# Optimization experiments

Measured on AMD Instinct MI355X. Metric: run time of the kernel, lower is better.

The kernel has to match this reference:

```python
import jax, jax.numpy as jnp
import numpy as np

N, E, D_IN, D_H, D_OUT = 100000, 1600000, 128, 128, 47
BN_EPS = 1e-5


def setup_inputs() -> dict:
    key = jax.random.key(0)
    ks = jax.random.split(key, 12)
    x = jax.random.normal(ks[0], (N, D_IN), dtype=jnp.float32)
    edge_index = jax.random.randint(ks[1], (2, E), 0, N, dtype=jnp.int64)
    s = 1.0 / np.sqrt(D_H)
    return {
        "x": x,
        "edge_index": edge_index,
        "W1": jax.random.normal(ks[2], (D_IN, D_H), dtype=jnp.float32) * s,
        "b1": jnp.zeros((D_H,), dtype=jnp.float32),
        "gamma": jax.random.uniform(ks[3], (D_H,), dtype=jnp.float32, minval=0.5, maxval=1.5),
        "beta": jax.random.normal(ks[4], (D_H,), dtype=jnp.float32) * 0.1,
        "mean": jax.random.normal(ks[5], (D_H,), dtype=jnp.float32) * 0.1,
        "var": jax.random.uniform(ks[6], (D_H,), dtype=jnp.float32, minval=0.5, maxval=1.5),
        "W2": jax.random.normal(ks[7], (D_H, D_H), dtype=jnp.float32) * s,
        "b2": jnp.zeros((D_H,), dtype=jnp.float32),
        "Wf": jax.random.normal(ks[8], (D_H, D_OUT), dtype=jnp.float32) * s,
        "bf": jnp.zeros((D_OUT,), dtype=jnp.float32),
    }


def gcn_conv(x, src, dst, W, b, n):
    # x' = x @ W, then symmetric-normalized aggregation with self-loops (PyG GCNConv).
    h = x @ W
    loops = jnp.arange(n, dtype=src.dtype)
    s = jnp.concatenate([src, loops])
    d = jnp.concatenate([dst, loops])
    deg = jax.ops.segment_sum(jnp.ones_like(d, dtype=h.dtype), d, num_segments=n)
    dinv = jnp.where(deg > 0, jax.lax.rsqrt(deg), 0.0)
    norm = dinv[s] * dinv[d]                      # [E+N]
    msg = h[s] * norm[:, None]                    # [E+N, D] gather
    out = jax.ops.segment_sum(msg, d, num_segments=n)  # scatter-add
    return out + b


def reference(x, edge_index, W1, b1, gamma, beta, mean, var, W2, b2, Wf, bf):
    n = x.shape[0]
    src, dst = edge_index[0], edge_index[1]
    # layer 1: GCNConv -> BatchNorm (eval) -> ReLU -> dropout (identity in eval)
    h1 = gcn_conv(x, src, dst, W1, b1, n)
    h1 = (h1 - mean) * jax.lax.rsqrt(var + BN_EPS) * gamma + beta
    h1 = jax.nn.relu(h1)
    # layer 2 (last conv, no BN/act)
    h2 = gcn_conv(h1, src, dst, W2, b2, n)
    # JumpingKnowledge max over layer outputs
    jk = jnp.maximum(h1, h2)
    logits = jk @ Wf + bf
    return jax.nn.log_softmax(logits, axis=1)
```

## Files before the change

kernel.cpp:

```cpp
#include <hip/hip_runtime.h>
#include <math.h>

#define DH 128
#define DOUT 47
#define BN_EPS 1e-5f

#define NCH 64
#define RS 32768
#define RSH 15

typedef __attribute__((ext_vector_type(8))) short short8;
typedef __attribute__((ext_vector_type(4))) float float4v;
typedef __attribute__((ext_vector_type(2))) float float2v;

__device__ __forceinline__ unsigned bf16_rne(float f) {
    unsigned u = __float_as_uint(f);
    return (u + 0x7fffu + ((u >> 16) & 1u)) >> 16;
}
__device__ __forceinline__ unsigned pack_bf2(float a, float b) {
    return (bf16_rne(a) & 0xffffu) | (bf16_rne(b) << 16);
}
__device__ __forceinline__ float2 unpack_bf2(unsigned u) {
    return make_float2(__uint_as_float(u << 16),
                       __uint_as_float(u & 0xffff0000u));
}


__global__ __launch_bounds__(256) void prep_k(const float* __restrict__ W1,
                                              const float* __restrict__ W2,
                                              unsigned* __restrict__ W1b,
                                              unsigned* __restrict__ W2b,
                                              unsigned* __restrict__ bufA, int n) {
    int tid = threadIdx.x;
    const float* W = blockIdx.x ? W2 : W1;
    unsigned* Wb = blockIdx.x ? W2b : W1b;
    if (blockIdx.x == 0 && tid < 64) bufA[(size_t)n * 64 + tid] = 0;
    for (int p = tid; p < 128 * 32; p += 256) {
        int nn = p >> 5;
        int k0 = (p & 31) << 2;
        float f0 = W[(size_t)(k0 + 0) * 128 + nn];
        float f1 = W[(size_t)(k0 + 1) * 128 + nn];
        float f2 = W[(size_t)(k0 + 2) * 128 + nn];
        float f3 = W[(size_t)(k0 + 3) * 128 + nn];
        uint2 v;
        v.x = pack_bf2(f0, f1);
        v.y = pack_bf2(f2, f3);
        *(uint2*)(Wb + (size_t)nn * 64 + (k0 >> 1)) = v;
    }
}

__global__ __launch_bounds__(256) void hist_rank_k(const int* __restrict__ dst,
                                                   int* __restrict__ rank,
                                                   int* __restrict__ cntM,
                                                   int e, int ce, int nr,
                                                   size_t nsp) {
    __shared__ int bins[RS];
    int tid = threadIdx.x;
    int r = blockIdx.x % nr;
    int ch = blockIdx.x / nr;
    {
        int4* b4 = (int4*)bins;
        for (int j = tid; j < RS / 4; j += 256) b4[j] = make_int4(0, 0, 0, 0);
    }
    __syncthreads();
    int lo = ch * ce;
    int hi = lo + ce;
    if (hi > e) hi = e;
    if (lo < hi) {
        int n4end = lo + ((hi - lo) & ~3);
        for (int i0 = lo + tid * 4; i0 < n4end; i0 += 1024) {
            int4 d4 = *(const int4*)(dst + i0);
            if ((d4.x >> RSH) == r) rank[i0 + 0] = atomicAdd(&bins[d4.x & (RS - 1)], 1);
            if ((d4.y >> RSH) == r) rank[i0 + 1] = atomicAdd(&bins[d4.y & (RS - 1)], 1);
            if ((d4.z >> RSH) == r) rank[i0 + 2] = atomicAdd(&bins[d4.z & (RS - 1)], 1);
            if ((d4.w >> RSH) == r) rank[i0 + 3] = atomicAdd(&bins[d4.w & (RS - 1)], 1);
        }
        for (int i0 = n4end + tid; i0 < hi; i0 += 256) {
            int d = dst[i0];
            if ((d >> RSH) == r) rank[i0] = atomicAdd(&bins[d & (RS - 1)], 1);
        }
    }
    __syncthreads();
    {
        int* outp = cntM + (size_t)ch * nsp + ((size_t)r << RSH);
        const int4* b4 = (const int4*)bins;
        int4* o4 = (int4*)outp;
        for (int j = tid; j < RS / 4; j += 256) o4[j] = b4[j];
    }
}

__global__ __launch_bounds__(256) void scan1_k(const int* __restrict__ cntM,
                                               int* __restrict__ counts,
                                               int* __restrict__ offsets,
                                               int* __restrict__ blocksums,
                                               size_t nsp, int n) {
    __shared__ int sd[256];
    int tid = threadIdx.x;
    int base = blockIdx.x * 1024 + tid * 4;
    int v[4];
#pragma unroll
    for (int j = 0; j < 4; j++) {
        int idx = base + j;
        int c = 0;
        if (idx < n) {
            for (int ch = 0; ch < NCH; ch++) c += cntM[(size_t)ch * nsp + idx];
            counts[idx] = c;
            c = (c + 7) & ~7;
        }
        v[j] = c;
    }
    int tsum = v[0] + v[1] + v[2] + v[3];
    sd[tid] = tsum;
    __syncthreads();
    for (int off = 1; off < 256; off <<= 1) {
        int x = (tid >= off) ? sd[tid - off] : 0;
        __syncthreads();
        sd[tid] += x;
        __syncthreads();
    }
    if (tid == 255) blocksums[blockIdx.x] = sd[255];
    int run = sd[tid] - tsum;
    if (base + 0 < n) offsets[base + 0] = run;  run += v[0];
    if (base + 1 < n) offsets[base + 1] = run;  run += v[1];
    if (base + 2 < n) offsets[base + 2] = run;  run += v[2];
    if (base + 3 < n) offsets[base + 3] = run;
}

__global__ __launch_bounds__(128) void scan2_k(int* __restrict__ blocksums, int nb,
                                               int* __restrict__ el, int n) {
    __shared__ int sd[128];
    int tid = threadIdx.x;
    int v = (tid < nb) ? blocksums[tid] : 0;
    sd[tid] = v;
    __syncthreads();
    for (int off = 1; off < 128; off <<= 1) {
        int x = (tid >= off) ? sd[tid - off] : 0;
        __syncthreads();
        sd[tid] += x;
        __syncthreads();
    }
    if (tid < nb) blocksums[tid] = sd[tid] - v;
    int total = sd[127];
    if (tid < 96) el[total + tid] = n;
}

__global__ void finalize_k(int* __restrict__ offsets,
                           float* __restrict__ dinv,
                           const int* __restrict__ counts,
                           const int* __restrict__ blocksums,
                           int* __restrict__ cntM,
                           int* __restrict__ el, size_t nsp, int n) {
    int i = blockIdx.x * 256 + threadIdx.x;
    if (i >= n) return;
    int o = offsets[i] + blocksums[i >> 10];
    offsets[i] = o;
    int run = o;
    for (int ch = 0; ch < NCH; ch++) {
        size_t idx = (size_t)ch * nsp + i;
        int c = cntM[idx];
        cntM[idx] = run;
        run += c;
    }
    int c = counts[i];
    dinv[i] = rsqrtf((float)(c + 1));
    int cP = (c + 7) & ~7;
    for (int j = o + c; j < o + cP; ++j) el[j] = n;
}

__global__ __launch_bounds__(256) void fused_sg_k(
    const float* __restrict__ A, const unsigned* __restrict__ Wb,
    unsigned* __restrict__ Cb, int M,
    const int* __restrict__ src, const int* __restrict__ dst,
    const int* __restrict__ rank, const int* __restrict__ baseM,
    const float* __restrict__ dinv, int* __restrict__ el,
    int e, int ce, size_t nsp, int gemmBlocks) {
    __shared__ ushort Bl[128 * 136];
    int bid = blockIdx.x;
    int q = bid >> 1;
    int tid = threadIdx.x;

    if (bid & 1) {
        int i0 = (q * 256 + tid) * 4;
        if (i0 + 4 <= e) {
            int4 s4 = *(const int4*)(src + i0);
            int4 d4 = *(const int4*)(dst + i0);
            int4 r4 = *(const int4*)(rank + i0);
            const int* bM = baseM + (size_t)(i0 / ce) * nsp;
            unsigned qx = (unsigned)(dinv[s4.x] * 32767.f + 0.5f);
            unsigned qy = (unsigned)(dinv[s4.y] * 32767.f + 0.5f);
            unsigned qz = (unsigned)(dinv[s4.z] * 32767.f + 0.5f);
            unsigned qw = (unsigned)(dinv[s4.w] * 32767.f + 0.5f);
            el[bM[d4.x] + r4.x] = (int)((unsigned)s4.x | (qx << 17));
            el[bM[d4.y] + r4.y] = (int)((unsigned)s4.y | (qy << 17));
            el[bM[d4.z] + r4.z] = (int)((unsigned)s4.z | (qz << 17));
            el[bM[d4.w] + r4.w] = (int)((unsigned)s4.w | (qw << 17));
        } else {
            for (int i = i0; i < e; i++) {
                unsigned qv = (unsigned)(dinv[src[i]] * 32767.f + 0.5f);
                int idx = baseM[(size_t)(i / ce) * nsp + dst[i]] + rank[i];
                el[idx] = (int)((unsigned)src[i] | (qv << 17));
            }
        }
        return;
    }

    if (q >= gemmBlocks) return;
    {
        unsigned* Bu = (unsigned*)Bl;
        for (int p = tid; p < 128 * 16; p += 256) {
            int row = p >> 4;
            int c = (p & 15) << 2;
            uint4 v = *(const uint4*)(Wb + (size_t)row * 64 + c);
            *(uint4*)(Bu + (size_t)row * 68 + c) = v;
        }
    }
    __syncthreads();

    int lane = tid & 63;
    int wv = tid >> 6;
    int quad = lane >> 4;
    int l15 = lane & 15;
    int r0 = q * 64 + wv * 16;
    int mload = r0 + l15;
    if (mload > M - 1) mload = M - 1;
    const float* Ar = A + (size_t)mload * 128 + quad * 8;

    float4v acc[8];
#pragma unroll
    for (int t = 0; t < 8; t++) acc[t] = (float4v){0.f, 0.f, 0.f, 0.f};

    for (int kp = 0; kp < 4; ++kp) {
        float4 a0 = *(const float4*)(Ar + kp * 32);
        float4 a1 = *(const float4*)(Ar + kp * 32 + 4);
        float af[8] = {a0.x, a0.y, a0.z, a0.w, a1.x, a1.y, a1.z, a1.w};
        short8 av;
#pragma unroll
        for (int j = 0; j < 8; j++) av[j] = (short)bf16_rne(af[j]);
        int kb = kp * 32 + quad * 8;
#pragma unroll
        for (int nt = 0; nt < 8; nt++) {
            short8 b8 = *(const short8*)(&Bl[(size_t)(nt * 16 + l15) * 136 + kb]);
            acc[nt] = __builtin_amdgcn_mfma_f32_16x16x32_bf16(av, b8, acc[nt], 0, 0, 0);
        }
    }

    ushort* Cu = (ushort*)Cb;
#pragma unroll
    for (int r = 0; r < 4; r++) {
        int row = r0 + quad * 4 + r;
        if (row < M) {
#pragma unroll
            for (int nt = 0; nt < 8; nt++) {
                Cu[(size_t)row * 128 + nt * 16 + l15] =
                    (ushort)bf16_rne(acc[nt][r]);
            }
        }
    }
}

__global__ __launch_bounds__(256) void gemm_bf16_k(const unsigned* __restrict__ Ab,
                                                   const unsigned* __restrict__ Wb,
                                                   unsigned* __restrict__ Cb, int M) {
    __shared__ ushort Bl[128 * 136];
    int tid = threadIdx.x;
    {
        unsigned* Bu = (unsigned*)Bl;
        for (int q = tid; q < 128 * 16; q += 256) {
            int row = q >> 4;
            int c = (q & 15) << 2;
            uint4 v = *(const uint4*)(Wb + (size_t)row * 64 + c);
            *(uint4*)(Bu + (size_t)row * 68 + c) = v;
        }
    }
    __syncthreads();

    int lane = tid & 63;
    int wv = tid >> 6;
    int quad = lane >> 4;
    int l15 = lane & 15;
    int r0 = blockIdx.x * 64 + wv * 16;
    int mload = r0 + l15;
    if (mload > M - 1) mload = M - 1;
    const unsigned* Ar = Ab + (size_t)mload * 64 + quad * 4;

    float4v acc[8];
#pragma unroll
    for (int t = 0; t < 8; t++) acc[t] = (float4v){0.f, 0.f, 0.f, 0.f};

    for (int kp = 0; kp < 4; ++kp) {
        uint4 a4 = *(const uint4*)(Ar + kp * 16);
        short8 av;
        av[0] = (short)(a4.x & 0xffff); av[1] = (short)(a4.x >> 16);
        av[2] = (short)(a4.y & 0xffff); av[3] = (short)(a4.y >> 16);
        av[4] = (short)(a4.z & 0xffff); av[5] = (short)(a4.z >> 16);
        av[6] = (short)(a4.w & 0xffff); av[7] = (short)(a4.w >> 16);
        int kb = kp * 32 + quad * 8;
#pragma unroll
        for (int nt = 0; nt < 8; nt++) {
            short8 b8 = *(const short8*)(&Bl[(size_t)(nt * 16 + l15) * 136 + kb]);
            acc[nt] = __builtin_amdgcn_mfma_f32_16x16x32_bf16(av, b8, acc[nt], 0, 0, 0);
        }
    }

    ushort* Cu = (ushort*)Cb;
#pragma unroll
    for (int r = 0; r < 4; r++) {
        int row = r0 + quad * 4 + r;
        if (row < M) {
#pragma unroll
            for (int nt = 0; nt < 8; nt++) {
                Cu[(size_t)row * 128 + nt * 16 + l15] =
                    (ushort)bf16_rne(acc[nt][r]);
            }
        }
    }
}

__device__ __forceinline__ float4 agg_core(const uint2* __restrict__ Hu2,
                                           const int* __restrict__ el,
                                           int start, int cnt, int node,
                                           float dvn, int li, int half) {
    float2v a01 = {0.f, 0.f};
    float2v a23 = {0.f, 0.f};
    int groups = ((cnt + 7) & ~7) >> 3;
    if (groups > 0) {
        const int* p = el + start + half * 4;

#define EDGE(cu, rr) {                                                       \
        float qf = (float)((unsigned)(rr) >> 17) * (1.f / 32767.f);          \
        float2v f0, f1;                                                      \
        f0.x = __uint_as_float((cu).x << 16);                                \
        f0.y = __uint_as_float((cu).x & 0xffff0000u);                        \
        f1.x = __uint_as_float((cu).y << 16);                                \
        f1.y = __uint_as_float((cu).y & 0xffff0000u);                        \
        a01.x = fmaf(f0.x, qf, a01.x); a01.y = fmaf(f0.y, qf, a01.y);        \
        a23.x = fmaf(f1.x, qf, a23.x); a23.y = fmaf(f1.y, qf, a23.y);        \
}
        int4 rc = *(const int4*)p;
        uint2 c0 = Hu2[(size_t)(rc.x & 0x1FFFF) * 32 + li];
        uint2 c1 = Hu2[(size_t)(rc.y & 0x1FFFF) * 32 + li];
        uint2 c2 = Hu2[(size_t)(rc.z & 0x1FFFF) * 32 + li];
        uint2 c3 = Hu2[(size_t)(rc.w & 0x1FFFF) * 32 + li];
        int4 rn = *(const int4*)(p + 8);
        for (int g = 0; g < groups; ++g) {
            uint2 n0 = Hu2[(size_t)(rn.x & 0x1FFFF) * 32 + li];
            uint2 n1 = Hu2[(size_t)(rn.y & 0x1FFFF) * 32 + li];
            uint2 n2 = Hu2[(size_t)(rn.z & 0x1FFFF) * 32 + li];
            uint2 n3 = Hu2[(size_t)(rn.w & 0x1FFFF) * 32 + li];
            int4 r2 = *(const int4*)(p + 8 * (g + 2));
            EDGE(c0, rc.x) EDGE(c1, rc.y) EDGE(c2, rc.z) EDGE(c3, rc.w)
            c0 = n0; c1 = n1; c2 = n2; c3 = n3;
            rc = rn; rn = r2;
        }
#undef EDGE
    }
    float4 acc = make_float4(a01.x, a01.y, a23.x, a23.y);
    acc.x += __shfl_xor(acc.x, 32);
    acc.y += __shfl_xor(acc.y, 32);
    acc.z += __shfl_xor(acc.z, 32);
    acc.w += __shfl_xor(acc.w, 32);
    uint2 sv = Hu2[(size_t)node * 32 + li];
    float2 s0 = unpack_bf2(sv.x);
    float2 s1 = unpack_bf2(sv.y);
    acc.x = fmaf(s0.x, dvn, acc.x); acc.y = fmaf(s0.y, dvn, acc.y);
    acc.z = fmaf(s1.x, dvn, acc.z); acc.w = fmaf(s1.y, dvn, acc.w);
    return acc;
}

__global__ __launch_bounds__(256) void agg1_k(
    const unsigned* __restrict__ H, const int* __restrict__ el,
    const int* __restrict__ offsets, const int* __restrict__ counts,
    const float* __restrict__ dinv, const float* __restrict__ b1,
    const float* __restrict__ gamma, const float* __restrict__ beta,
    const float* __restrict__ mean, const float* __restrict__ var,
    unsigned* __restrict__ H1b, int n) {
    int lane = threadIdx.x & 63;
    int li = lane & 31;
    int half = lane >> 5;
    int node = blockIdx.x * 4 + (threadIdx.x >> 6);
    if (node >= n) return;
    float dv = dinv[node];
    float4 acc = agg_core((const uint2*)H, el, offsets[node],
                          counts[node], node, dv, li, half);
    if (half == 0) {
        int f0 = li * 4;
        float4 bb = *(const float4*)(b1 + f0);
        float4 mm = *(const float4*)(mean + f0);
        float4 vv = *(const float4*)(var + f0);
        float4 gg = *(const float4*)(gamma + f0);
        float4 be = *(const float4*)(beta + f0);
        float4 o;
        o.x = fmaxf((acc.x * dv + bb.x - mm.x) * rsqrtf(vv.x + BN_EPS) * gg.x + be.x, 0.f);
        o.y = fmaxf((acc.y * dv + bb.y - mm.y) * rsqrtf(vv.y + BN_EPS) * gg.y + be.y, 0.f);
        o.z = fmaxf((acc.z * dv + bb.z - mm.z) * rsqrtf(vv.z + BN_EPS) * gg.z + be.z, 0.f);
        o.w = fmaxf((acc.w * dv + bb.w - mm.w) * rsqrtf(vv.w + BN_EPS) * gg.w + be.w, 0.f);
        uint2 pk;
        pk.x = pack_bf2(o.x, o.y);
        pk.y = pack_bf2(o.z, o.w);
        *(uint2*)(H1b + (size_t)node * 64 + li * 2) = pk;
    }
}

__global__ __launch_bounds__(256) void agg2_k(
    const unsigned* __restrict__ H, const int* __restrict__ el,
    const int* __restrict__ offsets, const int* __restrict__ counts,
    const float* __restrict__ dinv, const float* __restrict__ b2,
    unsigned* __restrict__ H1b, int n) {
    int lane = threadIdx.x & 63;
    int li = lane & 31;
    int half = lane >> 5;
    int node = blockIdx.x * 4 + (threadIdx.x >> 6);
    if (node >= n) return;
    float dv = dinv[node];
    float4 acc = agg_core((const uint2*)H, el, offsets[node],
                          counts[node], node, dv, li, half);
    if (half == 0) {
        int f0 = li * 4;
        float4 bb = *(const float4*)(b2 + f0);
        uint2* p = (uint2*)(H1b + (size_t)node * 64 + li * 2);
        uint2 hv = *p;
        float2 ha = unpack_bf2(hv.x);
        float2 hb = unpack_bf2(hv.y);
        float4 o;
        o.x = fmaxf(ha.x, acc.x * dv + bb.x);
        o.y = fmaxf(ha.y, acc.y * dv + bb.y);
        o.z = fmaxf(hb.x, acc.z * dv + bb.z);
        o.w = fmaxf(hb.y, acc.w * dv + bb.w);
        uint2 pk;
        pk.x = pack_bf2(o.x, o.y);
        pk.y = pack_bf2(o.z, o.w);
        *p = pk;
    }
}

__global__ __launch_bounds__(256) void head_k(const unsigned* __restrict__ JKb,
                                              const float* __restrict__ Wf,
                                              const float* __restrict__ bf,
                                              float* __restrict__ out, int n) {
    __shared__ __align__(16) float Bs[48 * 132];
    __shared__ __align__(16) float As[64 * 36];
    int tid = threadIdx.x;
    for (int p = tid; p < 47 * 32; p += 256) {
        int c = p >> 5;
        int k0 = (p & 31) << 2;
        float4 v;
        v.x = Wf[(size_t)(k0 + 0) * DOUT + c];
        v.y = Wf[(size_t)(k0 + 1) * DOUT + c];
        v.z = Wf[(size_t)(k0 + 2) * DOUT + c];
        v.w = Wf[(size_t)(k0 + 3) * DOUT + c];
        *(float4*)(&Bs[c * 132 + k0]) = v;
    }
    int tx = tid & 15;
    int ty = tid >> 4;
    int node0 = blockIdx.x * 64;

    float acc[4][3];
#pragma unroll
    for (int i = 0; i < 4; i++)
#pragma unroll
        for (int j = 0; j < 3; j++) acc[i][j] = 0.f;

    for (int kk = 0; kk < 128; kk += 32) {
        __syncthreads();
        for (int l = tid; l < 512; l += 256) {
            int r = l >> 3;
            int c4 = (l & 7) << 2;
            int row = node0 + r;
            float4 v = make_float4(0.f, 0.f, 0.f, 0.f);
            if (row < n) {
                uint2 u = *(const uint2*)(JKb + (size_t)row * 64 + ((kk + c4) >> 1));
                float2 f0 = unpack_bf2(u.x);
                float2 f1 = unpack_bf2(u.y);
                v = make_float4(f0.x, f0.y, f1.x, f1.y);
            }
            *(float4*)(&As[r * 36 + c4]) = v;
        }
        __syncthreads();
#pragma unroll
        for (int k4 = 0; k4 < 32; k4 += 4) {
            float4 a0 = *(const float4*)(&As[(ty * 4 + 0) * 36 + k4]);
            float4 a1 = *(const float4*)(&As[(ty * 4 + 1) * 36 + k4]);
            float4 a2 = *(const float4*)(&As[(ty * 4 + 2) * 36 + k4]);
            float4 a3 = *(const float4*)(&As[(ty * 4 + 3) * 36 + k4]);
            float4 b0 = *(const float4*)(&Bs[(tx * 3 + 0) * 132 + kk + k4]);
            float4 b1 = *(const float4*)(&Bs[(tx * 3 + 1) * 132 + kk + k4]);
            float4 b2 = *(const float4*)(&Bs[(tx * 3 + 2) * 132 + kk + k4]);
#define DOT_ROW(i, a)                                                        \
            acc[i][0] = fmaf(a.x, b0.x, acc[i][0]);                          \
            acc[i][0] = fmaf(a.y, b0.y, acc[i][0]);                          \
            acc[i][0] = fmaf(a.z, b0.z, acc[i][0]);                          \
            acc[i][0] = fmaf(a.w, b0.w, acc[i][0]);                          \
            acc[i][1] = fmaf(a.x, b1.x, acc[i][1]);                          \
            acc[i][1] = fmaf(a.y, b1.y, acc[i][1]);                          \
            acc[i][1] = fmaf(a.z, b1.z, acc[i][1]);                          \
            acc[i][1] = fmaf(a.w, b1.w, acc[i][1]);                          \
            acc[i][2] = fmaf(a.x, b2.x, acc[i][2]);                          \
            acc[i][2] = fmaf(a.y, b2.y, acc[i][2]);                          \
            acc[i][2] = fmaf(a.z, b2.z, acc[i][2]);                          \
            acc[i][2] = fmaf(a.w, b2.w, acc[i][2]);
            DOT_ROW(0, a0)
            DOT_ROW(1, a1)
            DOT_ROW(2, a2)
            DOT_ROW(3, a3)
#undef DOT_ROW
        }
    }

    float bfv[3];
#pragma unroll
    for (int j = 0; j < 3; j++) {
        int c = tx * 3 + j;
        bfv[j] = (c < DOUT) ? bf[c] : 0.f;
    }
#pragma unroll
    for (int i = 0; i < 4; i++) {
        int node = node0 + ty * 4 + i;
        float l0 = acc[i][0] + bfv[0];
        float l1 = acc[i][1] + bfv[1];
        float l2 = acc[i][2] + bfv[2];
        bool v2ok = (tx * 3 + 2) < DOUT;
        float m = fmaxf(l0, l1);
        if (v2ok) m = fmaxf(m, l2);
        for (int off = 8; off >= 1; off >>= 1) m = fmaxf(m, __shfl_xor(m, off));
        float s = expf(l0 - m) + expf(l1 - m) + (v2ok ? expf(l2 - m) : 0.f);
        for (int off = 8; off >= 1; off >>= 1) s += __shfl_xor(s, off);
        float ls = m + logf(s);
        if (node < n) {
            float* o = out + (size_t)node * DOUT + tx * 3;
            o[0] = l0 - ls;
            o[1] = l1 - ls;
            if (v2ok) o[2] = l2 - ls;
        }
    }
}

extern "C" void kernel_launch(void* const* d_in, const int* in_sizes, int n_in,
                              void* d_out, int out_size, void* d_ws, size_t ws_size,
                              hipStream_t stream) {
    const float* x     = (const float*)d_in[0];
    const int*   ei    = (const int*)d_in[1];
    const float* W1    = (const float*)d_in[2];
    const float* b1    = (const float*)d_in[3];
    const float* gamma = (const float*)d_in[4];
    const float* beta  = (const float*)d_in[5];
    const float* mean  = (const float*)d_in[6];
    const float* var   = (const float*)d_in[7];
    const float* W2    = (const float*)d_in[8];
    const float* b2    = (const float*)d_in[9];
    const float* Wf    = (const float*)d_in[10];
    const float* bf    = (const float*)d_in[11];
    float* out = (float*)d_out;

    int N_ = in_sizes[0] / 128;
    int E_ = in_sizes[1] / 2;
    const int* src = ei;
    const int* dst = ei + E_;

    int NR = (N_ + RS - 1) >> RSH;
    size_t NSP = (size_t)NR << RSH;
    int CE = ((E_ + NCH - 1) / NCH + 3) & ~3;

    char* ws = (char*)d_ws;
    unsigned* bufA = (unsigned*)ws; ws += (size_t)(N_ + 1) * 64 * 4;
    size_t h1bSz = (size_t)N_ * 64 * 4;
    size_t cntSz = (size_t)NCH * NSP * 4;
    unsigned* h1b = (unsigned*)ws;
    int* cntM     = (int*)ws;       ws += (h1bSz > cntSz ? h1bSz : cntSz);
    int*   counts  = (int*)ws;    ws += (size_t)N_ * 4;
    int*   offsets = (int*)ws;    ws += (size_t)N_ * 4;
    float* dinv    = (float*)ws;  ws += (size_t)N_ * 4;
    int*   rank    = (int*)ws;    ws += (size_t)E_ * 4;
    int*   el      = (int*)ws;    ws += ((size_t)E_ + 7 * (size_t)N_ + 128) * 4;
    int*   bsums   = (int*)ws;    ws += 1024 * 4;
    unsigned* W1b  = (unsigned*)ws; ws += 128 * 64 * 4;
    unsigned* W2b  = (unsigned*)ws; ws += 128 * 64 * 4;

    int nb = (N_ + 1023) / 1024;
    int gemmBlocks = (N_ + 63) / 64;
    int scatBlocks = (E_ + 1023) / 1024;
    int pairs = gemmBlocks > scatBlocks ? gemmBlocks : scatBlocks;

    prep_k<<<2, 256, 0, stream>>>(W1, W2, W1b, W2b, bufA, N_);
    hist_rank_k<<<NCH * NR, 256, 0, stream>>>(dst, rank, cntM, E_, CE, NR, NSP);
    scan1_k<<<nb, 256, 0, stream>>>(cntM, counts, offsets, bsums, NSP, N_);
    scan2_k<<<1, 128, 0, stream>>>(bsums, nb, el, N_);
    finalize_k<<<(N_ + 255) / 256, 256, 0, stream>>>(offsets, dinv, counts,
                                                     bsums, cntM, el, NSP, N_);
    fused_sg_k<<<2 * pairs, 256, 0, stream>>>(x, W1b, bufA, N_,
                                              src, dst, rank, cntM, dinv, el,
                                              E_, CE, NSP, gemmBlocks);
    agg1_k<<<(N_ + 3) / 4, 256, 0, stream>>>(bufA, el, offsets, counts, dinv,
                                             b1, gamma, beta, mean, var, h1b, N_);
    gemm_bf16_k<<<gemmBlocks, 256, 0, stream>>>(h1b, W2b, bufA, N_);
    agg2_k<<<(N_ + 3) / 4, 256, 0, stream>>>(bufA, el, offsets, counts, dinv,
                                             b2, h1b, N_);
    head_k<<<(N_ + 63) / 64, 256, 0, stream>>>(h1b, Wf, bf, out, N_);
}
```

Baseline: 415.8 us.

## Pre-fill edge list with sentinel in prep and halve GEMM LDS footprint

The edge list is now filled with the sentinel node index by extra blocks in the prep kernel using vectorized stores. This replaces the per-node padding loop in finalize and the tail write in scan2, removing divergent scalar writes from finalize. It costs a full pass of writes over the edge-list buffer. Separately, the fused GEMM stages the bf16 weight matrix into shared memory in two K-halves with an extra barrier, which halves shared memory per block to raise occupancy alongside the scatter blocks.

```diff
diff --git a/kernel.cpp b/kernel.cpp
--- a/kernel.cpp
+++ b/kernel.cpp
@@ -30,8 +30,14 @@
                                               const float* __restrict__ W2,
                                               unsigned* __restrict__ W1b,
                                               unsigned* __restrict__ W2b,
-                                              unsigned* __restrict__ bufA, int n) {
+                                              unsigned* __restrict__ bufA, int n,
+                                              int* __restrict__ el, int elsz4) {
     int tid = threadIdx.x;
+    if (blockIdx.x >= 2) {
+        int i4 = (blockIdx.x - 2) * 256 + tid;
+        if (i4 < elsz4) *(int4*)(el + (size_t)i4 * 4) = make_int4(n, n, n, n);
+        return;
+    }
     const float* W = blockIdx.x ? W2 : W1;
     unsigned* Wb = blockIdx.x ? W2b : W1b;
     if (blockIdx.x == 0 && tid < 64) bufA[(size_t)n * 64 + tid] = 0;
@@ -126,8 +132,7 @@
     if (base + 3 < n) offsets[base + 3] = run;
 }
 
-__global__ __launch_bounds__(128) void scan2_k(int* __restrict__ blocksums, int nb,
-                                               int* __restrict__ el, int n) {
+__global__ __launch_bounds__(128) void scan2_k(int* __restrict__ blocksums, int nb) {
     __shared__ int sd[128];
     int tid = threadIdx.x;
     int v = (tid < nb) ? blocksums[tid] : 0;
@@ -140,16 +145,13 @@
         __syncthreads();
     }
     if (tid < nb) blocksums[tid] = sd[tid] - v;
-    int total = sd[127];
-    if (tid < 96) el[total + tid] = n;
 }
 
 __global__ void finalize_k(int* __restrict__ offsets,
                            float* __restrict__ dinv,
                            const int* __restrict__ counts,
                            const int* __restrict__ blocksums,
-                           int* __restrict__ cntM,
-                           int* __restrict__ el, size_t nsp, int n) {
+                           int* __restrict__ cntM, size_t nsp, int n) {
     int i = blockIdx.x * 256 + threadIdx.x;
     if (i >= n) return;
     int o = offsets[i] + blocksums[i >> 10];
@@ -163,8 +165,6 @@
     }
     int c = counts[i];
     dinv[i] = rsqrtf((float)(c + 1));
-    int cP = (c + 7) & ~7;
-    for (int j = o + c; j < o + cP; ++j) el[j] = n;
 }
 
 __global__ __launch_bounds__(256) void fused_sg_k(
@@ -174,7 +174,7 @@
     const int* __restrict__ rank, const int* __restrict__ baseM,
     const float* __restrict__ dinv, int* __restrict__ el,
     int e, int ce, size_t nsp, int gemmBlocks) {
-    __shared__ ushort Bl[128 * 136];
+    __shared__ ushort Bl[128 * 72];
     int bid = blockIdx.x;
     int q = bid >> 1;
     int tid = threadIdx.x;
@@ -205,17 +205,6 @@
     }
 
     if (q >= gemmBlocks) return;
-    {
-        unsigned* Bu = (unsigned*)Bl;
-        for (int p = tid; p < 128 * 16; p += 256) {
-            int row = p >> 4;
-            int c = (p & 15) << 2;
-            uint4 v = *(const uint4*)(Wb + (size_t)row * 64 + c);
-            *(uint4*)(Bu + (size_t)row * 68 + c) = v;
-        }
-    }
-    __syncthreads();
-
     int lane = tid & 63;
     int wv = tid >> 6;
     int quad = lane >> 4;
@@ -229,18 +218,32 @@
 #pragma unroll
     for (int t = 0; t < 8; t++) acc[t] = (float4v){0.f, 0.f, 0.f, 0.f};
 
-    for (int kp = 0; kp < 4; ++kp) {
-        float4 a0 = *(const float4*)(Ar + kp * 32);
-        float4 a1 = *(const float4*)(Ar + kp * 32 + 4);
-        float af[8] = {a0.x, a0.y, a0.z, a0.w, a1.x, a1.y, a1.z, a1.w};
-        short8 av;
-#pragma unroll
-        for (int j = 0; j < 8; j++) av[j] = (short)bf16_rne(af[j]);
-        int kb = kp * 32 + quad * 8;
-#pragma unroll
-        for (int nt = 0; nt < 8; nt++) {
-            short8 b8 = *(const short8*)(&Bl[(size_t)(nt * 16 + l15) * 136 + kb]);
-            acc[nt] = __builtin_amdgcn_mfma_f32_16x16x32_bf16(av, b8, acc[nt], 0, 0, 0);
+    unsigned* Bu = (unsigned*)Bl;
+#pragma unroll
+    for (int ph = 0; ph < 2; ++ph) {
+        if (ph) __syncthreads();
+        for (int p = tid; p < 1024; p += 256) {
+            int row = p >> 3;
+            int c4 = (p & 7) << 2;
+            uint4 v = *(const uint4*)(Wb + (size_t)row * 64 + ph * 32 + c4);
+            *(uint4*)(Bu + (size_t)row * 36 + c4) = v;
+        }
+        __syncthreads();
+#pragma unroll
+        for (int kpl = 0; kpl < 2; ++kpl) {
+            int kp = ph * 2 + kpl;
+            float4 a0 = *(const float4*)(Ar + kp * 32);
+            float4 a1 = *(const float4*)(Ar + kp * 32 + 4);
+            float af[8] = {a0.x, a0.y, a0.z, a0.w, a1.x, a1.y, a1.z, a1.w};
+            short8 av;
+#pragma unroll
+            for (int j = 0; j < 8; j++) av[j] = (short)bf16_rne(af[j]);
+            int kb = kpl * 32 + quad * 8;
+#pragma unroll
+            for (int nt = 0; nt < 8; nt++) {
+                short8 b8 = *(const short8*)(&Bl[(size_t)(nt * 16 + l15) * 72 + kb]);
+                acc[nt] = __builtin_amdgcn_mfma_f32_16x16x32_bf16(av, b8, acc[nt], 0, 0, 0);
+            }
         }
     }
 
@@ -559,6 +562,8 @@
     int NR = (N_ + RS - 1) >> RSH;
     size_t NSP = (size_t)NR << RSH;
     int CE = ((E_ + NCH - 1) / NCH + 3) & ~3;
+    int elTotal = E_ + 7 * N_ + 128;
+    int elsz4 = (elTotal + 3) / 4;
 
     char* ws = (char*)d_ws;
     unsigned* bufA = (unsigned*)ws; ws += (size_t)(N_ + 1) * 64 * 4;
@@ -570,7 +575,7 @@
     int*   offsets = (int*)ws;    ws += (size_t)N_ * 4;
     float* dinv    = (float*)ws;  ws += (size_t)N_ * 4;
     int*   rank    = (int*)ws;    ws += (size_t)E_ * 4;
-    int*   el      = (int*)ws;    ws += ((size_t)E_ + 7 * (size_t)N_ + 128) * 4;
+    int*   el      = (int*)ws;    ws += ((size_t)elsz4 * 4) * 4;
     int*   bsums   = (int*)ws;    ws += 1024 * 4;
     unsigned* W1b  = (unsigned*)ws; ws += 128 * 64 * 4;
     unsigned* W2b  = (unsigned*)ws; ws += 128 * 64 * 4;
@@ -579,13 +584,14 @@
     int gemmBlocks = (N_ + 63) / 64;
     int scatBlocks = (E_ + 1023) / 1024;
     int pairs = gemmBlocks > scatBlocks ? gemmBlocks : scatBlocks;
-
-    prep_k<<<2, 256, 0, stream>>>(W1, W2, W1b, W2b, bufA, N_);
+    int prepBlocks = 2 + (elsz4 + 255) / 256;
+
+    prep_k<<<prepBlocks, 256, 0, stream>>>(W1, W2, W1b, W2b, bufA, N_, el, elsz4);
     hist_rank_k<<<NCH * NR, 256, 0, stream>>>(dst, rank, cntM, E_, CE, NR, NSP);
     scan1_k<<<nb, 256, 0, stream>>>(cntM, counts, offsets, bsums, NSP, N_);
-    scan2_k<<<1, 128, 0, stream>>>(bsums, nb, el, N_);
+    scan2_k<<<1, 128, 0, stream>>>(bsums, nb);
     finalize_k<<<(N_ + 255) / 256, 256, 0, stream>>>(offsets, dinv, counts,
-                                                     bsums, cntM, el, NSP, N_);
+                                                     bsums, cntM, NSP, N_);
     fused_sg_k<<<2 * pairs, 256, 0, stream>>>(x, W1b, bufA, N_,
                                               src, dst, rank, cntM, dinv, el,
                                               E_, CE, NSP, gemmBlocks);
```

Result: no change. 421.8 us (+1.4%).
